# Optimization experiments

Hardware: AMD Instinct MI355X
Metric: run time of the kernel (lower is better)

The kernel has to match this reference:

```python
import jax, jax.numpy as jnp
import numpy as np

NEG_SLOPE = 0.2  # negative_slope of LeakyReLU

def _leaky_relu(x):
    return jnp.where(x >= 0, x, NEG_SLOPE * x)

def setup_inputs() -> dict:
    key = jax.random.key(0)
    ks = jax.random.split(key, 8)
    n_s, n_t, n_edges = 100000, 25000, 1600000
    d_s_in = d_t_in = 256
    d_s_out = d_t_out = 256
    x_source = jax.random.normal(ks[0], (n_s, d_s_in), jnp.float32)
    x_target = jax.random.normal(ks[1], (n_t, d_t_in), jnp.float32)
    # sparse neighborhood N: [n_target, n_source], COO (row=target i, col=source j)
    edge_row = jax.random.randint(ks[2], (n_edges,), 0, n_t)
    edge_col = jax.random.randint(ks[3], (n_edges,), 0, n_s)
    n_vals = jax.random.uniform(ks[4], (n_edges,), jnp.float32)
    # learnable parameters (xavier-uniform-ish scale)
    w_s = jax.random.normal(ks[5], (d_s_in, d_t_out), jnp.float32) * 0.074  # [source_in, target_out]
    w_t = jax.random.normal(ks[6], (d_t_in, d_s_out), jnp.float32) * 0.074  # [target_in, source_out]
    att_weight = jax.random.normal(ks[7], (d_t_out + d_s_out,), jnp.float32) * 0.074
    return {"x_source": x_source, "x_target": x_target, "n_vals": n_vals,
            "w_s": w_s, "w_t": w_t, "att_weight": att_weight,
            "edge_row": edge_row, "edge_col": edge_col}

def reference(x_source, x_target, n_vals, w_s, w_t, att_weight, edge_row, edge_col):
    n_s = x_source.shape[0]
    n_t = x_target.shape[0]
    d_t_out = w_s.shape[1]  # target_out_channels (split point of att_weight)
    s_msg = x_source @ w_s  # [n_s, target_out]
    t_msg = x_target @ w_t  # [n_t, source_out]
    # e_ij = LeakyReLU([s_msg_j || t_msg_i] @ a); factor the linear part per node
    a1 = att_weight[:d_t_out]   # acts on s_msg part
    a2 = att_weight[d_t_out:]   # acts on t_msg part
    p_s = s_msg @ a1            # [n_s]
    p_t = t_msg @ a2            # [n_t]
    # f on the transposed edge (i'=source=col, j'=target=row) with permuted weight
    # [a2 || a1] gives p_t[row] + p_s[col]: identical per-edge scores as e.
    ev = _leaky_relu(p_s[edge_col] + p_t[edge_row])  # [E]
    # sparse_row_norm (softmax=False): divide by row sums
    rowsum_t = jax.ops.segment_sum(ev, edge_row, num_segments=n_t)  # rows of N
    rowsum_s = jax.ops.segment_sum(ev, edge_col, num_segments=n_s)  # rows of N^T
    att_s = ev / rowsum_t[edge_row]  # A_s, aligned with N
    att_t = ev / rowsum_s[edge_col]  # A_t, aligned with N^T
    # Hadamard with N values, then sparse-dense matmul (scatter-add)
    w_e = n_vals * att_s
    w_f = n_vals * att_t
    message_on_target = jax.ops.segment_sum(w_e[:, None] * s_msg[edge_col], edge_row, num_segments=n_t)  # Y_t
    message_on_source = jax.ops.segment_sum(w_f[:, None] * t_msg[edge_row], edge_col, num_segments=n_s)  # Y_s
    # update_func=None -> identity
    return message_on_source, message_on_target
```

## Files before the change

kernel.cpp:

```cpp
#include <hip/hip_runtime.h>

#define D 256

typedef float f32x4 __attribute__((ext_vector_type(4)));

#define PROWS 32
#define PSTRIDE (D + 4)

__global__ __launch_bounds__(256) void fused_p_all(
        const float* __restrict__ xs, const float* __restrict__ ws,
        float* __restrict__ ps, unsigned short* __restrict__ xbs, int n_s, int nblk_s,
        const float* __restrict__ xt, const float* __restrict__ wt,
        float* __restrict__ pt, unsigned short* __restrict__ xbt, int n_t,
        const float* __restrict__ att) {
    __shared__ float sbuf[PROWS][PSTRIDE];
    const float* X; const float* W; float* p; unsigned short* xb;
    int M, att_off, row0;
    if (blockIdx.x < (unsigned)nblk_s) {
        X = xs; W = ws; p = ps; xb = xbs; M = n_s; att_off = 0;
        row0 = blockIdx.x * PROWS;
    } else {
        X = xt; W = wt; p = pt; xb = xbt; M = n_t; att_off = D;
        row0 = (blockIdx.x - nblk_s) * PROWS;
    }
    const int tid = threadIdx.x;
    for (int idx = tid; idx < PROWS * (D / 4); idx += 256) {
        int r = idx >> 6;
        int c4 = (idx & 63) * 4;
        int grow = row0 + r;
        int srcrow = grow < M ? grow : M - 1;
        *reinterpret_cast<float4*>(&sbuf[r][c4]) =
            *reinterpret_cast<const float4*>(X + (size_t)srcrow * D + c4);
    }
    __syncthreads();

    if (xb) {
        const int half = tid >> 7;
        const int c2 = (tid & 127) * 2;
        for (int r = half; r < PROWS; r += 2) {
            int row = row0 + r;
            if (row < M) {
                unsigned int u0 = __float_as_uint(sbuf[r][c2]);
                unsigned int u1 = __float_as_uint(sbuf[r][c2 + 1]);
                u0 = (u0 + 0x7FFFu + ((u0 >> 16) & 1u)) >> 16;
                u1 = (u1 + 0x7FFFu + ((u1 >> 16) & 1u)) >> 16;
                unsigned int packed = (u1 << 16) | (u0 & 0xFFFFu);
                *reinterpret_cast<unsigned int*>(xb + (size_t)row * D + c2) = packed;
            }
        }
    }

    const int g = tid >> 6;
    const int l = tid & 63;
    const int r0 = g * 8;
    float acc[8][4];
    #pragma unroll
    for (int r = 0; r < 8; ++r)
        #pragma unroll
        for (int q = 0; q < 4; ++q) acc[r][q] = 0.f;

    const float* wbase = W + 4 * l;
    for (int k8 = 0; k8 < D; k8 += 8) {
        float4 wv[8];
        #pragma unroll
        for (int kk = 0; kk < 8; ++kk)
            wv[kk] = *reinterpret_cast<const float4*>(wbase + (size_t)(k8 + kk) * D);
        #pragma unroll
        for (int h = 0; h < 2; ++h) {
            float4 xv[8];
            #pragma unroll
            for (int r = 0; r < 8; ++r)
                xv[r] = *reinterpret_cast<const float4*>(&sbuf[r0 + r][k8 + 4 * h]);
            #pragma unroll
            for (int kk = 0; kk < 4; ++kk) {
                float4 w4 = wv[4 * h + kk];
                #pragma unroll
                for (int r = 0; r < 8; ++r) {
                    float xsc = (kk == 0) ? xv[r].x : (kk == 1) ? xv[r].y
                              : (kk == 2) ? xv[r].z : xv[r].w;
                    acc[r][0] = __fmaf_rn(xsc, w4.x, acc[r][0]);
                    acc[r][1] = __fmaf_rn(xsc, w4.y, acc[r][1]);
                    acc[r][2] = __fmaf_rn(xsc, w4.z, acc[r][2]);
                    acc[r][3] = __fmaf_rn(xsc, w4.w, acc[r][3]);
                }
            }
        }
    }
    __syncthreads();
    #pragma unroll
    for (int r = 0; r < 8; ++r)
        *reinterpret_cast<float4*>(&sbuf[r0 + r][4 * l]) =
            make_float4(acc[r][0], acc[r][1], acc[r][2], acc[r][3]);
    __syncthreads();
    if (tid < PROWS) {
        int row = row0 + tid;
        if (row < M) {
            float s = 0.f;
            const float* ap = att + att_off;
            for (int j = 0; j < D; ++j) s = __fmaf_rn(sbuf[tid][j], ap[j], s);
            p[row] = s;
        }
    }
}

__global__ void count_kernel(const int* __restrict__ er, const int* __restrict__ ec,
                             int* __restrict__ cnt_t, int* __restrict__ cnt_s, int ne) {
    int e = blockIdx.x * blockDim.x + threadIdx.x;
    int st = gridDim.x * blockDim.x;
    for (; e < ne; e += st) {
        atomicAdd(&cnt_t[er[e]], 1);
        atomicAdd(&cnt_s[ec[e]], 1);
    }
}

#define STILE 4096

__global__ __launch_bounds__(256) void scanA_kernel(
        const int* __restrict__ cnt_t, int n_t,
        const int* __restrict__ cnt_s, int n_s,
        int* __restrict__ tsum, int tilesT) {
    __shared__ int wsum[4];
    const int tid = threadIdx.x;
    const int* src; int n, base;
    if ((int)blockIdx.x < tilesT) { src = cnt_t; n = n_t; base = blockIdx.x * STILE; }
    else { src = cnt_s; n = n_s; base = (blockIdx.x - tilesT) * STILE; }
    int s = 0;
    for (int it = 0; it < STILE; it += 1024) {
        int idx = base + it + tid * 4;
        if (idx + 3 < n) {
            int4 v = *reinterpret_cast<const int4*>(src + idx);
            s += v.x + v.y + v.z + v.w;
        } else {
            #pragma unroll
            for (int k = 0; k < 4; ++k) if (idx + k < n) s += src[idx + k];
        }
    }
    #pragma unroll
    for (int o = 32; o > 0; o >>= 1) s += __shfl_xor(s, o, 64);
    if ((tid & 63) == 0) wsum[tid >> 6] = s;
    __syncthreads();
    if (tid == 0) tsum[blockIdx.x] = wsum[0] + wsum[1] + wsum[2] + wsum[3];
}

__global__ void scanB_kernel(int* __restrict__ tsum, int tilesT, int tilesS,
                             int* __restrict__ off_t, int n_t,
                             int* __restrict__ off_s, int n_s, int ne) {
    if (threadIdx.x == 0) {
        int run = 0;
        for (int i = 0; i < tilesT; ++i) { int v = tsum[i]; tsum[i] = run; run += v; }
        run = 0;
        for (int i = 0; i < tilesS; ++i) { int v = tsum[tilesT + i]; tsum[tilesT + i] = run; run += v; }
        off_t[n_t] = ne;
        off_s[n_s] = ne;
    }
}

__global__ __launch_bounds__(256) void scanC_kernel(
        const int* __restrict__ cnt_t, int n_t, int* __restrict__ off_t,
        const int* __restrict__ cnt_s, int n_s, int* __restrict__ off_s,
        const int* __restrict__ tsum, int tilesT) {
    __shared__ int wsum[4];
    __shared__ int s_carry;
    const int tid = threadIdx.x;
    const int lane = tid & 63, wv = tid >> 6;
    const int* src; int* dst; int n, base;
    if ((int)blockIdx.x < tilesT) { src = cnt_t; dst = off_t; n = n_t; base = blockIdx.x * STILE; }
    else { src = cnt_s; dst = off_s; n = n_s; base = (blockIdx.x - tilesT) * STILE; }
    if (tid == 0) s_carry = tsum[blockIdx.x];
    __syncthreads();
    for (int it = 0; it < STILE; it += 1024) {
        int idx = base + it + tid * 4;
        int4 v = make_int4(0, 0, 0, 0);
        if (idx + 3 < n) v = *reinterpret_cast<const int4*>(src + idx);
        else {
            if (idx < n)     v.x = src[idx];
            if (idx + 1 < n) v.y = src[idx + 1];
            if (idx + 2 < n) v.z = src[idx + 2];
        }
        int t4 = v.x + v.y + v.z + v.w;
        int x = t4;
        #pragma unroll
        for (int o = 1; o < 64; o <<= 1) {
            int y = __shfl_up(x, o, 64);
            if (lane >= o) x += y;
        }
        if (lane == 63) wsum[wv] = x;
        __syncthreads();
        int woff = 0;
        for (int w = 0; w < 4; ++w) if (w < wv) woff += wsum[w];
        int excl = s_carry + woff + x - t4;
        int4 outv;
        outv.x = excl;
        outv.y = excl + v.x;
        outv.z = excl + v.x + v.y;
        outv.w = excl + v.x + v.y + v.z;
        if (idx + 3 < n) *reinterpret_cast<int4*>(dst + idx) = outv;
        else {
            if (idx < n)     dst[idx] = outv.x;
            if (idx + 1 < n) dst[idx + 1] = outv.y;
            if (idx + 2 < n) dst[idx + 2] = outv.z;
        }
        __syncthreads();
        if (tid == 255) s_carry = excl + t4;
        __syncthreads();
    }
}

__global__ void fill_kernel(const int* __restrict__ er, const int* __restrict__ ec,
                            const int* __restrict__ off_t, const int* __restrict__ off_s,
                            int* __restrict__ cur_t, int* __restrict__ cur_s,
                            int* __restrict__ list_t, int* __restrict__ list_s, int ne) {
    int e = blockIdx.x * blockDim.x + threadIdx.x;
    int st = gridDim.x * blockDim.x;
    for (; e < ne; e += st) {
        int r = er[e];
        int p1 = atomicAdd(&cur_t[r], 1);
        list_t[off_t[r] + p1] = e;
        int c = ec[e];
        int p2 = atomicAdd(&cur_s[c], 1);
        list_s[off_s[c] + p2] = e;
    }
}

#define MAXD 160

__global__ __launch_bounds__(64) void rowsum_weight_all(
        const int* __restrict__ off_t, int* __restrict__ list_t,
        const int* __restrict__ ecol,
        const float* __restrict__ p_t, const float* __restrict__ p_s,
        float* __restrict__ wlist_t, int n_t,
        const int* __restrict__ off_s, int* __restrict__ list_s,
        const int* __restrict__ erow,
        float* __restrict__ wlist_s, int n_s,
        const float* __restrict__ nv) {
    __shared__ int raw[MAXD];
    __shared__ int so[MAXD];
    __shared__ float sev[MAXD];
    __shared__ float snv[MAXD];
    const int bid = blockIdx.x;
    const int* off; int* list; const int* other_idx;
    const float* p_own; const float* p_other; float* wlist; int row;
    if (bid < n_t) { off = off_t; list = list_t; other_idx = ecol;
                     p_own = p_t; p_other = p_s; wlist = wlist_t; row = bid; }
    else           { off = off_s; list = list_s; other_idx = erow;
                     p_own = p_s; p_other = p_t; wlist = wlist_s; row = bid - n_t; }
    const int lane = threadIdx.x;
    const int b = off[row];
    int deg = off[row + 1] - b;
    if (deg > MAXD) deg = MAXD;

    for (int i = lane; i < deg; i += 64)
        raw[i] = __builtin_nontemporal_load(list + b + i);
    __syncthreads();
    int myv[(MAXD + 63) / 64], myr[(MAXD + 63) / 64];
    #pragma unroll
    for (int c = 0; c < (MAXD + 63) / 64; ++c) {
        int i = lane + c * 64;
        if (i < deg) {
            int v = raw[i];
            int rank = 0;
            for (int j = 0; j < deg; ++j) rank += (raw[j] < v);
            myv[c] = v; myr[c] = rank;
        }
    }
    __syncthreads();
    #pragma unroll
    for (int c = 0; c < (MAXD + 63) / 64; ++c) {
        int i = lane + c * 64;
        if (i < deg) raw[myr[c]] = myv[c];
    }
    __syncthreads();
    const float po = p_own[row];
    for (int i = lane; i < deg; i += 64) {
        int e = raw[i];
        int o = other_idx[e];
        so[i] = o;
        float t = __fadd_rn(p_other[o], po);
        sev[i] = (t >= 0.f) ? t : __fmul_rn(0.2f, t);
        snv[i] = __builtin_nontemporal_load(nv + e);
    }
    __syncthreads();
    float rs = 0.f;
    for (int i = 0; i < deg; ++i) rs = __fadd_rn(rs, sev[i]);
    for (int i = lane; i < deg; i += 64) {
        list[b + i]  = so[i];
        wlist[b + i] = __fmul_rn(snv[i], __fdiv_rn(sev[i], rs));
    }
}

__global__ __launch_bounds__(256) void gather_all_bf16(
        const int* __restrict__ off_t, const int* __restrict__ olist_t,
        const float* __restrict__ wlist_t, const unsigned short* __restrict__ xb_s,
        float* __restrict__ out_tgt, int n_t,
        const int* __restrict__ off_s, const int* __restrict__ olist_s,
        const float* __restrict__ wlist_s, const unsigned short* __restrict__ xb_t,
        float* __restrict__ out_src, int n_s) {
    const int gid = blockIdx.x * 4 + (threadIdx.x >> 6);
    if (gid >= n_t + n_s) return;
    const int lane = threadIdx.x & 63;
    const int* off; const int* ol; const float* wl;
    const unsigned short* xo; float* out; int row;
    if (gid < n_t) { off = off_t; ol = olist_t; wl = wlist_t;
                     xo = xb_s; out = out_tgt; row = gid; }
    else           { off = off_s; ol = olist_s; wl = wlist_s;
                     xo = xb_t; out = out_src; row = gid - n_t; }
    const int b = off[row];
    const int end = off[row + 1];
    const size_t eoff = (size_t)lane * 4;

    float ax = 0.f, ay = 0.f, az = 0.f, aw = 0.f;
    for (int cs = b; cs < end; cs += 64) {
        const int cn = min(64, end - cs);
        int o_l = 0; float w_l = 0.f;
        if (lane < cn) {
            o_l = __builtin_nontemporal_load(ol + cs + lane);
            w_l = __builtin_nontemporal_load(wl + cs + lane);
        }
        int e = 0;
        for (; e + 16 <= cn; e += 16) {
            float w[16]; uint2 xv[16];
            #pragma unroll
            for (int u = 0; u < 16; ++u) {
                int o = __shfl(o_l, e + u, 64);
                w[u] = __shfl(w_l, e + u, 64);
                xv[u] = *reinterpret_cast<const uint2*>(xo + (size_t)o * D + eoff);
            }
            #pragma unroll
            for (int u = 0; u < 16; ++u) {
                float x0 = __uint_as_float(xv[u].x << 16);
                float x1 = __uint_as_float(xv[u].x & 0xFFFF0000u);
                float x2 = __uint_as_float(xv[u].y << 16);
                float x3 = __uint_as_float(xv[u].y & 0xFFFF0000u);
                ax = fmaf(w[u], x0, ax); ay = fmaf(w[u], x1, ay);
                az = fmaf(w[u], x2, az); aw = fmaf(w[u], x3, aw);
            }
        }
        for (; e < cn; ++e) {
            int o = __shfl(o_l, e, 64);
            float w = __shfl(w_l, e, 64);
            uint2 xv = *reinterpret_cast<const uint2*>(xo + (size_t)o * D + eoff);
            float x0 = __uint_as_float(xv.x << 16);
            float x1 = __uint_as_float(xv.x & 0xFFFF0000u);
            float x2 = __uint_as_float(xv.y << 16);
            float x3 = __uint_as_float(xv.y & 0xFFFF0000u);
            ax = fmaf(w, x0, ax); ay = fmaf(w, x1, ay);
            az = fmaf(w, x2, az); aw = fmaf(w, x3, aw);
        }
    }
    f32x4 r = {ax, ay, az, aw};
    __builtin_nontemporal_store(r,
        reinterpret_cast<f32x4*>(out + (size_t)row * D + eoff));
}

#define BAND 32
#define KT 8

__global__ __launch_bounds__(256) void band_gemm_all(
        float* __restrict__ Cs, const float* __restrict__ Bs_w, int nblk_s, int Ms,
        float* __restrict__ Ct, const float* __restrict__ Bt_w, int Mt) {
    __shared__ float Xs[BAND][D];
    __shared__ float Bs[KT][D];
    float* C; const float* B; int M, base_row;
    if (blockIdx.x < (unsigned)nblk_s) { C = Cs; B = Bs_w; M = Ms; base_row = blockIdx.x * BAND; }
    else { C = Ct; B = Bt_w; M = Mt; base_row = (blockIdx.x - nblk_s) * BAND; }
    const int tid = threadIdx.x;
    const int r0 = (tid >> 5) * 4;
    const int cA = (tid & 31) * 4;

    for (int s = tid; s < BAND * (D / 4); s += 256) {
        int row = s >> 6;
        int c4 = (s & 63) * 4;
        int grow = base_row + row;
        int srow = grow < M ? grow : M - 1;
        f32x4 v = __builtin_nontemporal_load(
            reinterpret_cast<const f32x4*>(C + (size_t)srow * D + c4));
        *reinterpret_cast<f32x4*>(&Xs[row][c4]) = v;
    }

    float acc[4][8];
    #pragma unroll
    for (int i = 0; i < 4; ++i)
        #pragma unroll
        for (int j = 0; j < 8; ++j) acc[i][j] = 0.f;

    for (int kt = 0; kt < D; kt += KT) {
        __syncthreads();
        for (int s = tid; s < KT * (D / 4); s += 256) {
            int row = s >> 6;
            int c4 = (s & 63) * 4;
            *reinterpret_cast<float4*>(&Bs[row][c4]) =
                *reinterpret_cast<const float4*>(B + (size_t)(kt + row) * D + c4);
        }
        __syncthreads();
        #pragma unroll
        for (int k4 = 0; k4 < KT; k4 += 4) {
            float4 av[4];
            #pragma unroll
            for (int i = 0; i < 4; ++i)
                av[i] = *reinterpret_cast<const float4*>(&Xs[r0 + i][kt + k4]);
            #pragma unroll
            for (int kk = 0; kk < 4; ++kk) {
                float4 blo = *reinterpret_cast<const float4*>(&Bs[k4 + kk][cA]);
                float4 bhi = *reinterpret_cast<const float4*>(&Bs[k4 + kk][cA + 128]);
                #pragma unroll
                for (int i = 0; i < 4; ++i) {
                    float a = (kk == 0) ? av[i].x : (kk == 1) ? av[i].y
                            : (kk == 2) ? av[i].z : av[i].w;
                    acc[i][0] = fmaf(a, blo.x, acc[i][0]);
                    acc[i][1] = fmaf(a, blo.y, acc[i][1]);
                    acc[i][2] = fmaf(a, blo.z, acc[i][2]);
                    acc[i][3] = fmaf(a, blo.w, acc[i][3]);
                    acc[i][4] = fmaf(a, bhi.x, acc[i][4]);
                    acc[i][5] = fmaf(a, bhi.y, acc[i][5]);
                    acc[i][6] = fmaf(a, bhi.z, acc[i][6]);
                    acc[i][7] = fmaf(a, bhi.w, acc[i][7]);
                }
            }
        }
    }
    #pragma unroll
    for (int i = 0; i < 4; ++i) {
        int row = base_row + r0 + i;
        if (row < M) {
            float* cp = C + (size_t)row * D;
            f32x4 lo = {acc[i][0], acc[i][1], acc[i][2], acc[i][3]};
            f32x4 hi = {acc[i][4], acc[i][5], acc[i][6], acc[i][7]};
            __builtin_nontemporal_store(lo, reinterpret_cast<f32x4*>(cp + cA));
            __builtin_nontemporal_store(hi, reinterpret_cast<f32x4*>(cp + cA + 128));
        }
    }
}

extern "C" void kernel_launch(void* const* d_in, const int* in_sizes, int n_in,
                              void* d_out, int out_size, void* d_ws, size_t ws_size,
                              hipStream_t stream) {
    const float* x_s = (const float*)d_in[0];
    const float* x_t = (const float*)d_in[1];
    const float* nv  = (const float*)d_in[2];
    const float* w_s = (const float*)d_in[3];
    const float* w_t = (const float*)d_in[4];
    const float* att = (const float*)d_in[5];
    const int* erow  = (const int*)d_in[6];
    const int* ecol  = (const int*)d_in[7];

    const int n_s = in_sizes[0] / D;
    const int n_t = in_sizes[1] / D;
    const int ne  = in_sizes[6];

    float* p_s      = (float*)d_ws;
    float* p_t      = p_s + n_s;
    float* wlist_t  = p_t + n_t;
    float* wlist_s  = wlist_t + ne;
    int* cnt_t  = (int*)(wlist_s + ne);
    int* cnt_s  = cnt_t + n_t;
    int* cur_t  = cnt_s + n_s;
    int* cur_s  = cur_t + n_t;
    int* off_t  = cur_s + n_s;
    int* off_s  = off_t + (n_t + 1);
    int* tsum   = off_s + (n_s + 1);
    int* list_t = tsum + 64;
    int* list_s = list_t + ne;
    unsigned short* xb_s = (unsigned short*)(list_s + ne);
    unsigned short* xb_t = xb_s + (size_t)n_s * D;
    size_t need = (size_t)((char*)(xb_t + (size_t)n_t * D) - (char*)d_ws);
    const bool use_bf16 = ws_size >= need;

    float* out_src = (float*)d_out;
    float* out_tgt = out_src + (size_t)n_s * D;

    (void)hipMemsetAsync(cnt_t, 0, 2 * (size_t)(n_t + n_s) * sizeof(int), stream);

    const int pblk_s = (n_s + PROWS - 1) / PROWS;
    const int pblk_t = (n_t + PROWS - 1) / PROWS;
    fused_p_all<<<pblk_s + pblk_t, 256, 0, stream>>>(
        x_s, w_s, p_s, use_bf16 ? xb_s : nullptr, n_s, pblk_s,
        x_t, w_t, p_t, use_bf16 ? xb_t : nullptr, n_t, att);

    count_kernel<<<2048, 256, 0, stream>>>(erow, ecol, cnt_t, cnt_s, ne);

    const int tilesT = (n_t + STILE - 1) / STILE;
    const int tilesS = (n_s + STILE - 1) / STILE;
    scanA_kernel<<<tilesT + tilesS, 256, 0, stream>>>(cnt_t, n_t, cnt_s, n_s,
                                                      tsum, tilesT);
    scanB_kernel<<<1, 64, 0, stream>>>(tsum, tilesT, tilesS,
                                       off_t, n_t, off_s, n_s, ne);
    scanC_kernel<<<tilesT + tilesS, 256, 0, stream>>>(cnt_t, n_t, off_t,
                                                      cnt_s, n_s, off_s,
                                                      tsum, tilesT);

    fill_kernel<<<2048, 256, 0, stream>>>(erow, ecol, off_t, off_s, cur_t, cur_s,
                                          list_t, list_s, ne);

    rowsum_weight_all<<<n_t + n_s, 64, 0, stream>>>(off_t, list_t, ecol, p_t, p_s,
                                                    wlist_t, n_t,
                                                    off_s, list_s, erow,
                                                    wlist_s, n_s, nv);

    if (use_bf16) {
        int rows = n_t + n_s;
        gather_all_bf16<<<(rows + 3) / 4, 256, 0, stream>>>(
            off_t, list_t, wlist_t, xb_s, out_tgt, n_t,
            off_s, list_s, wlist_s, xb_t, out_src, n_s);
    }

    const int gblk_s = (n_s + BAND - 1) / BAND;
    const int gblk_t = (n_t + BAND - 1) / BAND;
    band_gemm_all<<<gblk_s + gblk_t, 256, 0, stream>>>(out_src, w_t, gblk_s, n_s,
                                                       out_tgt, w_s, n_t);
}
```

Measured before the change: 1.150 ms.

## Store gathered aggregates as bf16 and run output projection on MFMA

```diff
diff --git a/kernel.cpp b/kernel.cpp
--- a/kernel.cpp
+++ b/kernel.cpp
@@ -3,6 +3,14 @@
 #define D 256
 
 typedef float f32x4 __attribute__((ext_vector_type(4)));
+typedef unsigned int u32x2 __attribute__((ext_vector_type(2)));
+typedef short bf16x8 __attribute__((ext_vector_type(8)));
+typedef float floatx4 __attribute__((ext_vector_type(4)));
+
+__device__ __forceinline__ unsigned int rne_bf16(float f) {
+    unsigned int u = __float_as_uint(f);
+    return (u + 0x7FFFu + ((u >> 16) & 1u)) >> 16;
+}
 
 #define PROWS 32
 #define PSTRIDE (D + 4)
@@ -40,12 +48,10 @@
         for (int r = half; r < PROWS; r += 2) {
             int row = row0 + r;
             if (row < M) {
-                unsigned int u0 = __float_as_uint(sbuf[r][c2]);
-                unsigned int u1 = __float_as_uint(sbuf[r][c2 + 1]);
-                u0 = (u0 + 0x7FFFu + ((u0 >> 16) & 1u)) >> 16;
-                u1 = (u1 + 0x7FFFu + ((u1 >> 16) & 1u)) >> 16;
-                unsigned int packed = (u1 << 16) | (u0 & 0xFFFFu);
-                *reinterpret_cast<unsigned int*>(xb + (size_t)row * D + c2) = packed;
+                unsigned int u0 = rne_bf16(sbuf[r][c2]);
+                unsigned int u1 = rne_bf16(sbuf[r][c2 + 1]);
+                *reinterpret_cast<unsigned int*>(xb + (size_t)row * D + c2) =
+                    (u1 << 16) | u0;
             }
         }
     }
@@ -291,19 +297,19 @@
 __global__ __launch_bounds__(256) void gather_all_bf16(
         const int* __restrict__ off_t, const int* __restrict__ olist_t,
         const float* __restrict__ wlist_t, const unsigned short* __restrict__ xb_s,
-        float* __restrict__ out_tgt, int n_t,
+        float* __restrict__ out_tgt, unsigned short* __restrict__ aggb_tgt, int n_t,
         const int* __restrict__ off_s, const int* __restrict__ olist_s,
         const float* __restrict__ wlist_s, const unsigned short* __restrict__ xb_t,
-        float* __restrict__ out_src, int n_s) {
+        float* __restrict__ out_src, unsigned short* __restrict__ aggb_src, int n_s) {
     const int gid = blockIdx.x * 4 + (threadIdx.x >> 6);
     if (gid >= n_t + n_s) return;
     const int lane = threadIdx.x & 63;
     const int* off; const int* ol; const float* wl;
-    const unsigned short* xo; float* out; int row;
+    const unsigned short* xo; float* out; unsigned short* aggb; int row;
     if (gid < n_t) { off = off_t; ol = olist_t; wl = wlist_t;
-                     xo = xb_s; out = out_tgt; row = gid; }
+                     xo = xb_s; out = out_tgt; aggb = aggb_tgt; row = gid; }
     else           { off = off_s; ol = olist_s; wl = wlist_s;
-                     xo = xb_t; out = out_src; row = gid - n_t; }
+                     xo = xb_t; out = out_src; aggb = aggb_src; row = gid - n_t; }
     const int b = off[row];
     const int end = off[row + 1];
     const size_t eoff = (size_t)lane * 4;
@@ -347,9 +353,70 @@
             az = fmaf(w, x2, az); aw = fmaf(w, x3, aw);
         }
     }
-    f32x4 r = {ax, ay, az, aw};
-    __builtin_nontemporal_store(r,
-        reinterpret_cast<f32x4*>(out + (size_t)row * D + eoff));
+    if (aggb) {
+        u32x2 pk = { (rne_bf16(ay) << 16) | rne_bf16(ax),
+                     (rne_bf16(aw) << 16) | rne_bf16(az) };
+        __builtin_nontemporal_store(pk,
+            reinterpret_cast<u32x2*>(aggb + (size_t)row * D + eoff));
+    } else {
+        f32x4 r = {ax, ay, az, aw};
+        __builtin_nontemporal_store(r,
+            reinterpret_cast<f32x4*>(out + (size_t)row * D + eoff));
+    }
+}
+
+#define GR 64
+
+__global__ __launch_bounds__(256) void band_mfma_all(
+        const unsigned short* __restrict__ aggb_s, float* __restrict__ out_s,
+        int nblk_s, int Ms, const float* __restrict__ W_for_s,
+        const unsigned short* __restrict__ aggb_t, float* __restrict__ out_t,
+        int Mt, const float* __restrict__ W_for_t) {
+    __shared__ unsigned short WT[256][40];
+    const unsigned short* A; float* Cout; const float* W; int M, base;
+    if (blockIdx.x < (unsigned)nblk_s) {
+        A = aggb_s; Cout = out_s; W = W_for_s; M = Ms; base = blockIdx.x * GR;
+    } else {
+        A = aggb_t; Cout = out_t; W = W_for_t; M = Mt;
+        base = (blockIdx.x - nblk_s) * GR;
+    }
+    const int tid = threadIdx.x;
+    const int wv = tid >> 6;
+    const int l  = tid & 63;
+    const int lr = l & 15;
+    const int lg = l >> 4;
+    const int wrow0 = base + wv * 16;
+
+    floatx4 acc[16];
+    #pragma unroll
+    for (int ct = 0; ct < 16; ++ct) acc[ct] = (floatx4){0.f, 0.f, 0.f, 0.f};
+
+    for (int ks = 0; ks < 8; ++ks) {
+        const int k0 = ks * 32;
+        __syncthreads();
+        for (int idx = tid; idx < 32 * 256; idx += 256) {
+            int c = idx & 255, kr = idx >> 8;
+            WT[c][kr] = (unsigned short)rne_bf16(W[(size_t)(k0 + kr) * D + c]);
+        }
+        __syncthreads();
+        int arow = wrow0 + lr;
+        if (arow >= M) arow = M - 1;
+        bf16x8 af = *reinterpret_cast<const bf16x8*>(A + (size_t)arow * D + k0 + 8 * lg);
+        #pragma unroll
+        for (int ct = 0; ct < 16; ++ct) {
+            bf16x8 bf = *reinterpret_cast<const bf16x8*>(&WT[ct * 16 + lr][8 * lg]);
+            acc[ct] = __builtin_amdgcn_mfma_f32_16x16x32_bf16(af, bf, acc[ct], 0, 0, 0);
+        }
+    }
+    #pragma unroll
+    for (int ct = 0; ct < 16; ++ct) {
+        int col = ct * 16 + lr;
+        #pragma unroll
+        for (int j = 0; j < 4; ++j) {
+            int row = wrow0 + lg * 4 + j;
+            if (row < M) Cout[(size_t)row * D + col] = acc[ct][j];
+        }
+    }
 }
 
 #define BAND 32
@@ -462,8 +529,12 @@
     int* list_s = list_t + ne;
     unsigned short* xb_s = (unsigned short*)(list_s + ne);
     unsigned short* xb_t = xb_s + (size_t)n_s * D;
-    size_t need = (size_t)((char*)(xb_t + (size_t)n_t * D) - (char*)d_ws);
-    const bool use_bf16 = ws_size >= need;
+    unsigned short* aggb_src = xb_t + (size_t)n_t * D;
+    unsigned short* aggb_tgt = aggb_src + (size_t)n_s * D;
+    size_t need_bf16 = (size_t)((char*)(xb_t + (size_t)n_t * D) - (char*)d_ws);
+    size_t need_mfma = (size_t)((char*)(aggb_tgt + (size_t)n_t * D) - (char*)d_ws);
+    const bool use_bf16 = ws_size >= need_bf16;
+    const bool use_mfma = ws_size >= need_mfma;
 
     float* out_src = (float*)d_out;
     float* out_tgt = out_src + (size_t)n_s * D;
@@ -496,15 +567,21 @@
                                                     off_s, list_s, erow,
                                                     wlist_s, n_s, nv);
 
-    if (use_bf16) {
-        int rows = n_t + n_s;
-        gather_all_bf16<<<(rows + 3) / 4, 256, 0, stream>>>(
-            off_t, list_t, wlist_t, xb_s, out_tgt, n_t,
-            off_s, list_s, wlist_s, xb_t, out_src, n_s);
-    }
-
-    const int gblk_s = (n_s + BAND - 1) / BAND;
-    const int gblk_t = (n_t + BAND - 1) / BAND;
-    band_gemm_all<<<gblk_s + gblk_t, 256, 0, stream>>>(out_src, w_t, gblk_s, n_s,
-                                                       out_tgt, w_s, n_t);
-}
+    int rows = n_t + n_s;
+    gather_all_bf16<<<(rows + 3) / 4, 256, 0, stream>>>(
+        off_t, list_t, wlist_t, xb_s, out_tgt, use_mfma ? aggb_tgt : nullptr, n_t,
+        off_s, list_s, wlist_s, xb_t, out_src, use_mfma ? aggb_src : nullptr, n_s);
+
+    if (use_mfma) {
+        const int mblk_s = (n_s + GR - 1) / GR;
+        const int mblk_t = (n_t + GR - 1) / GR;
+        band_mfma_all<<<mblk_s + mblk_t, 256, 0, stream>>>(
+            aggb_src, out_src, mblk_s, n_s, w_t,
+            aggb_tgt, out_tgt, n_t, w_s);
+    } else {
+        const int gblk_s = (n_s + BAND - 1) / BAND;
+        const int gblk_t = (n_t + BAND - 1) / BAND;
+        band_gemm_all<<<gblk_s + gblk_t, 256, 0, stream>>>(out_src, w_t, gblk_s, n_s,
+                                                           out_tgt, w_s, n_t);
+    }
+}
```

Result: faster. 994.6 us, median of 2 (-13.5%).
